# Kernel tuning notes

Measured on AMD Instinct MI355X. Metric: run time of the kernel, lower is better.

Reference implementation:

```python
import jax, jax.numpy as jnp
import numpy as np
from jax import lax

B, T, I, H, N = 8192, 100, 24, 64, 8  # batch, seq_len, input_size, hidden_size, hidden_neurons
H2 = 2 * H


def setup_inputs() -> dict:
    key = jax.random.key(0)
    ks = iter(jax.random.split(key, 80))
    d = {"input_seq": jax.random.normal(next(ks), (B, T, I), jnp.float32)}
    def triple(name, shape):
        d[name + "_mu"] = 0.1 * jax.random.normal(next(ks), shape, jnp.float32)
        d[name + "_rho"] = -6.0 + 0.1 * jax.random.normal(next(ks), shape, jnp.float32)
        d[name + "_eps"] = jax.random.normal(next(ks), shape, jnp.float32)
    # BayesianLSTM params: weight_ih (in, 4H), weight_hh (H, 4H), bias (4H,)
    triple("l1_wih", (I, 4 * H)); triple("l1_whh", (H, 4 * H)); triple("l1_b", (4 * H,))
    triple("l2_wih", (H, 4 * H2)); triple("l2_whh", (H2, 4 * H2)); triple("l2_b", (4 * H2,))
    # BayesianLinear params: weight (out, in), bias (out,)
    triple("fc1_w", (N, H2)); triple("fc1_b", (N,))
    triple("fc2_w", (N, N)); triple("fc2_b", (N,))
    triple("out_w", (1, N)); triple("out_b", (1,))
    return d


def _sample(mu, rho, eps):
    # blitz reparameterization: sigma = log1p(exp(rho))
    return mu + jnp.log1p(jnp.exp(rho)) * eps


def _lstm(x, wih, whh, b):
    # x: [B, T, in]; returns full hidden sequence [B, T, Hn]; gate order i,f,g,o
    Hn = whh.shape[0]
    xg = jnp.einsum('bti,ig->btg', x, wih) + b  # precompute input projection
    def step(carry, xg_t):
        h, c = carry
        gates = xg_t + h @ whh
        i, f, g, o = jnp.split(gates, 4, axis=-1)
        c = jax.nn.sigmoid(f) * c + jax.nn.sigmoid(i) * jnp.tanh(g)
        h = jax.nn.sigmoid(o) * jnp.tanh(c)
        return (h, c), h
    h0 = jnp.zeros((x.shape[0], Hn), x.dtype)
    _, hs = lax.scan(step, (h0, h0), jnp.swapaxes(xg, 0, 1))
    return jnp.swapaxes(hs, 0, 1)


def _forward(input_seq,
             l1_wih_mu, l1_wih_rho, l1_wih_eps, l1_whh_mu, l1_whh_rho, l1_whh_eps,
             l1_b_mu, l1_b_rho, l1_b_eps,
             l2_wih_mu, l2_wih_rho, l2_wih_eps, l2_whh_mu, l2_whh_rho, l2_whh_eps,
             l2_b_mu, l2_b_rho, l2_b_eps,
             fc1_w_mu, fc1_w_rho, fc1_w_eps, fc1_b_mu, fc1_b_rho, fc1_b_eps,
             fc2_w_mu, fc2_w_rho, fc2_w_eps, fc2_b_mu, fc2_b_rho, fc2_b_eps,
             out_w_mu, out_w_rho, out_w_eps, out_b_mu, out_b_rho, out_b_eps):
    w1i = _sample(l1_wih_mu, l1_wih_rho, l1_wih_eps)
    w1h = _sample(l1_whh_mu, l1_whh_rho, l1_whh_eps)
    b1 = _sample(l1_b_mu, l1_b_rho, l1_b_eps)
    w2i = _sample(l2_wih_mu, l2_wih_rho, l2_wih_eps)
    w2h = _sample(l2_whh_mu, l2_whh_rho, l2_whh_eps)
    b2 = _sample(l2_b_mu, l2_b_rho, l2_b_eps)
    fc1w = _sample(fc1_w_mu, fc1_w_rho, fc1_w_eps); fc1b = _sample(fc1_b_mu, fc1_b_rho, fc1_b_eps)
    fc2w = _sample(fc2_w_mu, fc2_w_rho, fc2_w_eps); fc2b = _sample(fc2_b_mu, fc2_b_rho, fc2_b_eps)
    outw = _sample(out_w_mu, out_w_rho, out_w_eps); outb = _sample(out_b_mu, out_b_rho, out_b_eps)

    h1 = _lstm(input_seq, w1i, w1h, b1)      # [B, T, H]
    h2 = _lstm(h1, w2i, w2h, b2)             # [B, T, 2H]
    out = h2[:, -1, :]                       # [B, 2H]
    x = jax.nn.relu(out @ fc1w.T + fc1b)
    x = jax.nn.relu(x @ fc2w.T + fc2b)
    y = x @ outw.T + outb                    # [B, 1]
    return y.reshape(-1)


def reference(input_seq,
              l1_wih_mu, l1_wih_rho, l1_wih_eps, l1_whh_mu, l1_whh_rho, l1_whh_eps,
              l1_b_mu, l1_b_rho, l1_b_eps,
              l2_wih_mu, l2_wih_rho, l2_wih_eps, l2_whh_mu, l2_whh_rho, l2_whh_eps,
              l2_b_mu, l2_b_rho, l2_b_eps,
              fc1_w_mu, fc1_w_rho, fc1_w_eps, fc1_b_mu, fc1_b_rho, fc1_b_eps,
              fc2_w_mu, fc2_w_rho, fc2_w_eps, fc2_b_mu, fc2_b_rho, fc2_b_eps,
              out_w_mu, out_w_rho, out_w_eps, out_b_mu, out_b_rho, out_b_eps):
    return _forward(input_seq,
                    l1_wih_mu, l1_wih_rho, l1_wih_eps, l1_whh_mu, l1_whh_rho, l1_whh_eps,
                    l1_b_mu, l1_b_rho, l1_b_eps,
                    l2_wih_mu, l2_wih_rho, l2_wih_eps, l2_whh_mu, l2_whh_rho, l2_whh_eps,
                    l2_b_mu, l2_b_rho, l2_b_eps,
                    fc1_w_mu, fc1_w_rho, fc1_w_eps, fc1_b_mu, fc1_b_rho, fc1_b_eps,
                    fc2_w_mu, fc2_w_rho, fc2_w_eps, fc2_b_mu, fc2_b_rho, fc2_b_eps,
                    out_w_mu, out_w_rho, out_w_eps, out_b_mu, out_b_rho, out_b_eps)
```

## Files before the change

kernel.cpp:

```cpp
#include <hip/hip_runtime.h>
#include <math.h>


typedef __attribute__((ext_vector_type(8))) short short8;
typedef __attribute__((ext_vector_type(4))) float f32x4;

#define MFMA16(a, b, c) __builtin_amdgcn_mfma_f32_16x16x32_bf16((a), (b), (c), 0, 0, 0)

#define WS_W1G_OFF 196608
#define WS_WF_OFF  245760

struct SampParams {
  const float* w1i[3]; const float* w1h[3]; const float* b1[3];
  const float* w2i[3]; const float* w2h[3]; const float* b2[3];
  const float* f1w[3]; const float* f1b[3];
  const float* f2w[3]; const float* f2b[3];
  const float* ow[3];  const float* ob[3];
  short* W2S; short* W1G; float* WF;
};

struct LstmParams {
  const float* input;
  const short* W2S; const short* W1G; const float* WF;
  float* out;
};

__device__ __forceinline__ float softplus_fast(float x) {
  float e = __builtin_amdgcn_exp2f(1.44269504f * x);
  return 0.69314718f * __builtin_amdgcn_logf(1.0f + e);
}

__device__ __forceinline__ float samp(const float* const q[3], int idx) {
  return q[0][idx] + softplus_fast(q[1][idx]) * q[2][idx];
}

__device__ __forceinline__ short f2bf(float f) {
  unsigned u = __float_as_uint(f);
  unsigned r = (u + 0x7FFFu + ((u >> 16) & 1u)) >> 16;
  return (short)r;
}

__device__ __forceinline__ unsigned cvt_pk_bf16(float lo, float hi) {
  unsigned r;
  asm("v_cvt_pk_bf16_f32 %0, %1, %2" : "=v"(r) : "v"(lo), "v"(hi));
  return r;
}

__device__ __forceinline__ void lstm_elem(float gi, float gf, float gg, float go,
                                          float& c, float& h) {
  float A = 1.0f + __builtin_amdgcn_exp2f(-1.44269504f * gi);
  float B = 1.0f + __builtin_amdgcn_exp2f(-1.44269504f * gf);
  float r = __builtin_amdgcn_rcpf(A * B);
  float si = r * B;
  float sf = r * A;
  float C = 1.0f + __builtin_amdgcn_exp2f(2.88539008f * gg);
  float D = 1.0f + __builtin_amdgcn_exp2f(-1.44269504f * go);
  float r2 = __builtin_amdgcn_rcpf(C * D);
  float tg = 1.0f - 2.0f * (r2 * D);
  float so = r2 * C;
  float cn = sf * c + si * tg;
  c = cn;
  float E = 1.0f + __builtin_amdgcn_exp2f(2.88539008f * cn);
  h = so * (1.0f - 2.0f * __builtin_amdgcn_rcpf(E));
}

__global__ __launch_bounds__(256) void sample_kernel(SampParams p)
{
  int i = blockIdx.x * 256 + threadIdx.x;
  if (i < 12288) {
    int tid = i & 511, gg = (i >> 9) & 3, kk = i >> 11;
    int quad = (tid >> 4) & 3, col = tid & 15, v0 = (tid >> 6) * 16;
    int c = gg * 128 + v0 + col;
    short8 v;
#pragma unroll
    for (int j = 0; j < 8; ++j) {
      int k = kk * 32 + quad * 8 + j;
      float x = (k < 64) ? samp(p.w2i, k * 512 + c) : samp(p.w2h, (k - 64) * 512 + c);
      v[j] = f2bf(x);
    }
    *(short8*)&p.W2S[i * 8] = v;
  } else if (i < 15360) {
    int u = i - 12288;
    int slice = u >> 8, n = u & 255;
    int k0 = (slice >> 2) * 32 + (slice & 3) * 8;
    short8 v;
#pragma unroll
    for (int j = 0; j < 8; ++j) {
      int k = k0 + j;
      float x = 0.0f;
      if (k < 24)       x = samp(p.w1i, k * 256 + n);
      else if (k >= 32) x = samp(p.w1h, (k - 32) * 256 + n);
      v[j] = f2bf(x);
    }
    *(short8*)&p.W1G[u * 8] = v;
  } else if (i < 17241) {
    int u = i - 15360;
    float x;
    if (u < 256)       x = samp(p.b1,  u);
    else if (u < 768)  x = samp(p.b2,  u - 256);
    else if (u < 1792) x = samp(p.f1w, u - 768);
    else if (u < 1856) x = samp(p.f2w, u - 1792);
    else if (u < 1864) x = samp(p.f1b, u - 1856);
    else if (u < 1872) x = samp(p.f2b, u - 1864);
    else if (u < 1880) x = samp(p.ow,  u - 1872);
    else               x = samp(p.ob,  0);
    p.WF[u] = x;
  }
}


__global__ __launch_bounds__(512, 2)
void blstm_kernel(LstmParams p)
{
  __shared__ __align__(16) unsigned char pool[79872];
  short* const W1L = (short*)pool;
  short* const A1b = (short*)(pool + 49152);
  short* const A2b = (short*)(pool + 62464);

  const int tid  = threadIdx.x;
  const int w    = tid >> 6;
  const int l    = tid & 63;
  const int quad = l >> 4;
  const int col  = l & 15;
  const int b0   = blockIdx.x * 32;

  const int wq = w & 3;
  const int mh = w >> 2;
  const int v0 = w * 16;

  const short8* const W2v = (const short8*)p.W2S;
  short8 w2r[24];
#pragma unroll
  for (int f = 0; f < 24; ++f) w2r[f] = W2v[f * 512 + tid];

#pragma unroll
  for (int r = 0; r < 6; ++r) {
    short8 v = *(const short8*)&p.W1G[(r * 512 + tid) * 8];
    *(short8*)&W1L[(r * 512 + tid) * 8] = v;
  }

  float b1v[4], b2v[4];
#pragma unroll
  for (int g = 0; g < 4; ++g) b1v[g] = p.WF[g * 64 + wq * 16 + col];
#pragma unroll
  for (int g = 0; g < 4; ++g) b2v[g] = p.WF[256 + g * 128 + v0 + col];

  for (int i = tid; i < 6656; i += 512) A1b[i] = 0;
  for (int i = tid; i < 8704; i += 512) A2b[i] = 0;
  __syncthreads();

  int xr = 0, xi = 0;
  const bool xln = tid < 384;
  const float* xptr = p.input;
  if (xln) {
    int e = tid * 2; xr = e / 24; xi = e - xr * 24;
    const float* base = p.input + (size_t)(b0 + xr) * 2400 + xi;
    float2 xv = *(const float2*)base;
    *(unsigned*)&A1b[xr * 104 + xi] = cvt_pk_bf16(xv.x, xv.y);
    xptr = base + 24;
  }
  __syncthreads();

  float c1a[4]  = {0.f, 0.f, 0.f, 0.f};
  float c2a[2][4] = {{0.f,0.f,0.f,0.f},{0.f,0.f,0.f,0.f}};
  float hf2[2][4];

  const int a1rd = (mh * 16 + col) * 104;

  auto step = [&](const short* __restrict__ A1r, const short* __restrict__ A2r,
                  short* __restrict__ A1w, short* __restrict__ A2w, bool dox) {
    const bool do_x = dox && xln;
    float2 xv;
    if (do_x) xv = *(const float2*)xptr;

    short8 aA0 = *(const short8*)&A1r[a1rd +      quad * 8];
    short8 aA1 = *(const short8*)&A1r[a1rd + 32 + quad * 8];
    short8 aA2 = *(const short8*)&A1r[a1rd + 64 + quad * 8];
    f32x4 g1[4];
#pragma unroll
    for (int g = 0; g < 4; ++g) {
      f32x4 acc = (f32x4){b1v[g], b1v[g], b1v[g], b1v[g]};
      acc = MFMA16(aA0, *(const short8*)&W1L[(((0 * 4 + quad) << 8) + g * 64 + wq * 16 + col) * 8], acc);
      acc = MFMA16(aA1, *(const short8*)&W1L[(((1 * 4 + quad) << 8) + g * 64 + wq * 16 + col) * 8], acc);
      acc = MFMA16(aA2, *(const short8*)&W1L[(((2 * 4 + quad) << 8) + g * 64 + wq * 16 + col) * 8], acc);
      g1[g] = acc;
    }

    {
      float h1v[4];
#pragma unroll
      for (int i = 0; i < 4; ++i)
        lstm_elem(g1[0][i], g1[1][i], g1[2][i], g1[3][i], c1a[i], h1v[i]);
      int base = (mh * 16 + quad * 4) * 104 + 32 + wq * 16 + col;
      unsigned pkA = cvt_pk_bf16(h1v[0], h1v[1]);
      unsigned pkB = cvt_pk_bf16(h1v[2], h1v[3]);
      A1w[base]       = (short)pkA;
      A1w[base + 104] = (short)(pkA >> 16);
      A1w[base + 208] = (short)pkB;
      A1w[base + 312] = (short)(pkB >> 16);
    }
    if (do_x)
      *(unsigned*)&A1w[xr * 104 + xi] = cvt_pk_bf16(xv.x, xv.y);

    f32x4 g2[2][4];
#pragma unroll
    for (int g = 0; g < 4; ++g) {
      g2[0][g] = (f32x4){b2v[g], b2v[g], b2v[g], b2v[g]};
      g2[1][g] = g2[0][g];
    }
#pragma unroll
    for (int kk = 0; kk < 6; ++kk) {
      short8 a0, a1f;
      if (kk < 2) {
        a0  = *(const short8*)&A1r[      col  * 104 + 32 + kk * 32 + quad * 8];
        a1f = *(const short8*)&A1r[(16 + col) * 104 + 32 + kk * 32 + quad * 8];
      } else {
        int o = (kk - 2) * 32 + quad * 8;
        a0  = *(const short8*)&A2r[      col  * 136 + o];
        a1f = *(const short8*)&A2r[(16 + col) * 136 + o];
      }
#pragma unroll
      for (int g = 0; g < 4; ++g) {
        g2[0][g] = MFMA16(a0,  w2r[kk * 4 + g], g2[0][g]);
        g2[1][g] = MFMA16(a1f, w2r[kk * 4 + g], g2[1][g]);
      }
    }

    {
      int u2 = v0 + col;
#pragma unroll
      for (int mi = 0; mi < 2; ++mi) {
        float hv[4];
#pragma unroll
        for (int i = 0; i < 4; ++i) {
          lstm_elem(g2[mi][0][i], g2[mi][1][i], g2[mi][2][i], g2[mi][3][i],
                    c2a[mi][i], hv[i]);
          hf2[mi][i] = hv[i];
        }
        unsigned pkA = cvt_pk_bf16(hv[0], hv[1]);
        unsigned pkB = cvt_pk_bf16(hv[2], hv[3]);
        int base = (mi * 16 + quad * 4) * 136 + u2;
        A2w[base]       = (short)pkA;
        A2w[base + 136] = (short)(pkA >> 16);
        A2w[base + 272] = (short)pkB;
        A2w[base + 408] = (short)(pkB >> 16);
      }
    }
  };

  short* const A1_0 = A1b;            short* const A1_1 = A1b + 3328;
  short* const A2_0 = A2b;            short* const A2_1 = A2b + 4352;

  {
    float2 xv;
    if (xln) xv = *(const float2*)xptr;
    short8 aA0 = *(const short8*)&A1_0[a1rd +      quad * 8];
    short8 aA1 = *(const short8*)&A1_0[a1rd + 32 + quad * 8];
    short8 aA2 = *(const short8*)&A1_0[a1rd + 64 + quad * 8];
    f32x4 g1[4];
#pragma unroll
    for (int g = 0; g < 4; ++g) {
      f32x4 acc = (f32x4){b1v[g], b1v[g], b1v[g], b1v[g]};
      acc = MFMA16(aA0, *(const short8*)&W1L[(((0 * 4 + quad) << 8) + g * 64 + wq * 16 + col) * 8], acc);
      acc = MFMA16(aA1, *(const short8*)&W1L[(((1 * 4 + quad) << 8) + g * 64 + wq * 16 + col) * 8], acc);
      acc = MFMA16(aA2, *(const short8*)&W1L[(((2 * 4 + quad) << 8) + g * 64 + wq * 16 + col) * 8], acc);
      g1[g] = acc;
    }
    float h1v[4];
#pragma unroll
    for (int i = 0; i < 4; ++i)
      lstm_elem(g1[0][i], g1[1][i], g1[2][i], g1[3][i], c1a[i], h1v[i]);
    int base = (mh * 16 + quad * 4) * 104 + 32 + wq * 16 + col;
    unsigned pkA = cvt_pk_bf16(h1v[0], h1v[1]);
    unsigned pkB = cvt_pk_bf16(h1v[2], h1v[3]);
    A1_1[base]       = (short)pkA;
    A1_1[base + 104] = (short)(pkA >> 16);
    A1_1[base + 208] = (short)pkB;
    A1_1[base + 312] = (short)(pkB >> 16);
    if (xln)
      *(unsigned*)&A1_1[xr * 104 + xi] = cvt_pk_bf16(xv.x, xv.y);
    __syncthreads();
    xptr += 24;
  }

  for (int jj = 1; jj <= 99; jj += 2) {
    step(A1_1, A2_1, A1_0, A2_0, jj <= 98);
    __syncthreads();
    xptr += 24;
    step(A1_0, A2_0, A1_1, A2_1, jj + 1 <= 98);
    __syncthreads();
    xptr += 24;
  }

  float* const H2   = (float*)pool;
  float* const FC1W = (float*)(pool + 16896);
  float* const FC2W = (float*)(pool + 20992);
  float* const FB1  = (float*)(pool + 21248);
  float* const FB2  = (float*)(pool + 21280);
  float* const OWp  = (float*)(pool + 21312);
  float* const OBp  = (float*)(pool + 21344);
  float* const X1   = (float*)(pool + 21376);
  float* const X2   = (float*)(pool + 22400);

  {
    int u2 = v0 + col;
#pragma unroll
    for (int mi = 0; mi < 2; ++mi)
#pragma unroll
      for (int i = 0; i < 4; ++i) {
        int row = mi * 16 + quad * 4 + i;
        H2[row * 132 + u2] = hf2[mi][i];
      }
  }
  for (int i = tid; i < 1024; i += 512) FC1W[i] = p.WF[768 + i];
  if (tid < 64)               FC2W[tid]     = p.WF[1792 + tid];
  if (tid >= 64 && tid < 72)  FB1[tid - 64] = p.WF[1856 + tid - 64];
  if (tid >= 72 && tid < 80)  FB2[tid - 72] = p.WF[1864 + tid - 72];
  if (tid >= 80 && tid < 88)  OWp[tid - 80] = p.WF[1872 + tid - 80];
  if (tid == 88)              OBp[0]        = p.WF[1880];
  __syncthreads();

  if (tid < 256) {
    int row = tid >> 3, o = tid & 7;
    float s = FB1[o];
#pragma unroll 8
    for (int k = 0; k < 128; ++k) s += H2[row * 132 + k] * FC1W[o * 128 + k];
    X1[tid] = fmaxf(s, 0.0f);
  }
  __syncthreads();
  if (tid < 256) {
    int row = tid >> 3, o = tid & 7;
    float s = FB2[o];
#pragma unroll
    for (int k = 0; k < 8; ++k) s += X1[row * 8 + k] * FC2W[o * 8 + k];
    X2[tid] = fmaxf(s, 0.0f);
  }
  __syncthreads();
  if (tid < 32) {
    float s = OBp[0];
#pragma unroll
    for (int k = 0; k < 8; ++k) s += X2[tid * 8 + k] * OWp[k];
    p.out[b0 + tid] = s;
  }
}

extern "C" void kernel_launch(void* const* d_in, const int* in_sizes, int n_in,
                              void* d_out, int out_size, void* d_ws, size_t ws_size,
                              hipStream_t stream)
{
  (void)in_sizes; (void)n_in; (void)ws_size; (void)out_size;

  SampParams sp;
  const float** grp[12] = { sp.w1i, sp.w1h, sp.b1, sp.w2i, sp.w2h, sp.b2,
                            sp.f1w, sp.f1b, sp.f2w, sp.f2b, sp.ow, sp.ob };
  int idx = 1;
  for (int t = 0; t < 12; ++t)
    for (int j = 0; j < 3; ++j)
      grp[t][j] = (const float*)d_in[idx++];
  sp.W2S = (short*)d_ws;
  sp.W1G = (short*)((char*)d_ws + WS_W1G_OFF);
  sp.WF  = (float*)((char*)d_ws + WS_WF_OFF);

  LstmParams bp;
  bp.input = (const float*)d_in[0];
  bp.W2S = (const short*)d_ws;
  bp.W1G = (const short*)((char*)d_ws + WS_W1G_OFF);
  bp.WF  = (const float*)((char*)d_ws + WS_WF_OFF);
  bp.out = (float*)d_out;

  sample_kernel<<<dim3(68), dim3(256), 0, stream>>>(sp);
  blstm_kernel<<<dim3(256), dim3(512), 0, stream>>>(bp);
}
```

Before: 400.0 us.

## Prefetch input one step ahead, batch LSTM reciprocals, use LDS-only barriers

Input loads for timestep t+1 are now issued one step early and written the following step, so global-load latency is hidden behind a full recurrence step. The LSTM cell math is restructured to share one reciprocal across all four gates and one across pairs of tanh(c), which cuts transcendental ops on the serial critical path. The cell state is clamped before the exp to avoid overflow. __syncthreads is replaced with an asm barrier that waits only on lgkmcnt, so the barrier does not stall on outstanding global loads. The risks are lower accuracy from the combined reciprocals and a correctness dependence on the custom barrier.

Result: slower. 410.0 us (+2.5%).

```diff
diff --git a/kernel.cpp b/kernel.cpp
--- a/kernel.cpp
+++ b/kernel.cpp
@@ -6,6 +6,8 @@
 typedef __attribute__((ext_vector_type(4))) float f32x4;
 
 #define MFMA16(a, b, c) __builtin_amdgcn_mfma_f32_16x16x32_bf16((a), (b), (c), 0, 0, 0)
+
+#define BARRIER() asm volatile("s_waitcnt lgkmcnt(0)\n\ts_barrier" ::: "memory")
 
 #define WS_W1G_OFF 196608
 #define WS_WF_OFF  245760
@@ -46,22 +48,35 @@
   return r;
 }
 
-__device__ __forceinline__ void lstm_elem(float gi, float gf, float gg, float go,
-                                          float& c, float& h) {
-  float A = 1.0f + __builtin_amdgcn_exp2f(-1.44269504f * gi);
-  float B = 1.0f + __builtin_amdgcn_exp2f(-1.44269504f * gf);
-  float r = __builtin_amdgcn_rcpf(A * B);
-  float si = r * B;
-  float sf = r * A;
-  float C = 1.0f + __builtin_amdgcn_exp2f(2.88539008f * gg);
-  float D = 1.0f + __builtin_amdgcn_exp2f(-1.44269504f * go);
-  float r2 = __builtin_amdgcn_rcpf(C * D);
-  float tg = 1.0f - 2.0f * (r2 * D);
-  float so = r2 * C;
-  float cn = sf * c + si * tg;
-  c = cn;
-  float E = 1.0f + __builtin_amdgcn_exp2f(2.88539008f * cn);
-  h = so * (1.0f - 2.0f * __builtin_amdgcn_rcpf(E));
+__device__ __forceinline__ void lstm_quad(const f32x4 gi, const f32x4 gf,
+                                          const f32x4 gg, const f32x4 go,
+                                          float* c, float* h) {
+  float E[4], so[4];
+#pragma unroll
+  for (int i = 0; i < 4; ++i) {
+    float a  = __builtin_amdgcn_exp2f(-1.44269504f * gi[i]);
+    float b  = __builtin_amdgcn_exp2f(-1.44269504f * gf[i]);
+    float cv = __builtin_amdgcn_exp2f( 2.88539008f * gg[i]);
+    float d  = __builtin_amdgcn_exp2f(-1.44269504f * go[i]);
+    float A = 1.0f + a, B = 1.0f + b, C = 1.0f + cv, D = 1.0f + d;
+    float P = A * B, Q = C * D;
+    float R = __builtin_amdgcn_rcpf(P * Q);
+    float RQ = R * Q, RP = R * P;
+    float si = RQ * B;
+    float sf = RQ * A;
+    float tg = 1.0f - 2.0f * (RP * D);
+    so[i]    = RP * C;
+    float cn = sf * c[i] + si * tg;
+    c[i] = cn;
+    float cc = fminf(fmaxf(cn, -15.0f), 15.0f);
+    E[i] = 1.0f + __builtin_amdgcn_exp2f(2.88539008f * cc);
+  }
+  float R01 = __builtin_amdgcn_rcpf(E[0] * E[1]);
+  float R23 = __builtin_amdgcn_rcpf(E[2] * E[3]);
+  h[0] = so[0] * (1.0f - 2.0f * (R01 * E[1]));
+  h[1] = so[1] * (1.0f - 2.0f * (R01 * E[0]));
+  h[2] = so[2] * (1.0f - 2.0f * (R23 * E[3]));
+  h[3] = so[3] * (1.0f - 2.0f * (R23 * E[2]));
 }
 
 __global__ __launch_bounds__(256) void sample_kernel(SampParams p)
@@ -155,23 +170,24 @@
   if (xln) {
     int e = tid * 2; xr = e / 24; xi = e - xr * 24;
     const float* base = p.input + (size_t)(b0 + xr) * 2400 + xi;
-    float2 xv = *(const float2*)base;
-    *(unsigned*)&A1b[xr * 104 + xi] = cvt_pk_bf16(xv.x, xv.y);
+    float2 xv0 = *(const float2*)base;
+    *(unsigned*)&A1b[xr * 104 + xi] = cvt_pk_bf16(xv0.x, xv0.y);
     xptr = base + 24;
   }
   __syncthreads();
 
-  float c1a[4]  = {0.f, 0.f, 0.f, 0.f};
+  float c1a[4]    = {0.f, 0.f, 0.f, 0.f};
   float c2a[2][4] = {{0.f,0.f,0.f,0.f},{0.f,0.f,0.f,0.f}};
   float hf2[2][4];
 
+  float2 xv_w, xv_n;
+
   const int a1rd = (mh * 16 + col) * 104;
 
   auto step = [&](const short* __restrict__ A1r, const short* __restrict__ A2r,
-                  short* __restrict__ A1w, short* __restrict__ A2w, bool dox) {
-    const bool do_x = dox && xln;
-    float2 xv;
-    if (do_x) xv = *(const float2*)xptr;
+                  short* __restrict__ A1w, short* __restrict__ A2w,
+                  bool w_x, bool l_x) {
+    if (l_x && xln) xv_n = *(const float2*)xptr;
 
     short8 aA0 = *(const short8*)&A1r[a1rd +      quad * 8];
     short8 aA1 = *(const short8*)&A1r[a1rd + 32 + quad * 8];
@@ -188,9 +204,7 @@
 
     {
       float h1v[4];
-#pragma unroll
-      for (int i = 0; i < 4; ++i)
-        lstm_elem(g1[0][i], g1[1][i], g1[2][i], g1[3][i], c1a[i], h1v[i]);
+      lstm_quad(g1[0], g1[1], g1[2], g1[3], c1a, h1v);
       int base = (mh * 16 + quad * 4) * 104 + 32 + wq * 16 + col;
       unsigned pkA = cvt_pk_bf16(h1v[0], h1v[1]);
       unsigned pkB = cvt_pk_bf16(h1v[2], h1v[3]);
@@ -199,8 +213,8 @@
       A1w[base + 208] = (short)pkB;
       A1w[base + 312] = (short)(pkB >> 16);
     }
-    if (do_x)
-      *(unsigned*)&A1w[xr * 104 + xi] = cvt_pk_bf16(xv.x, xv.y);
+    if (w_x && xln)
+      *(unsigned*)&A1w[xr * 104 + xi] = cvt_pk_bf16(xv_w.x, xv_w.y);
 
     f32x4 g2[2][4];
 #pragma unroll
@@ -231,12 +245,9 @@
 #pragma unroll
       for (int mi = 0; mi < 2; ++mi) {
         float hv[4];
-#pragma unroll
-        for (int i = 0; i < 4; ++i) {
-          lstm_elem(g2[mi][0][i], g2[mi][1][i], g2[mi][2][i], g2[mi][3][i],
-                    c2a[mi][i], hv[i]);
-          hf2[mi][i] = hv[i];
-        }
+        lstm_quad(g2[mi][0], g2[mi][1], g2[mi][2], g2[mi][3], c2a[mi], hv);
+#pragma unroll
+        for (int i = 0; i < 4; ++i) hf2[mi][i] = hv[i];
         unsigned pkA = cvt_pk_bf16(hv[0], hv[1]);
         unsigned pkB = cvt_pk_bf16(hv[2], hv[3]);
         int base = (mi * 16 + quad * 4) * 136 + u2;
@@ -246,14 +257,17 @@
         A2w[base + 408] = (short)(pkB >> 16);
       }
     }
+    xv_w = xv_n;
   };
 
   short* const A1_0 = A1b;            short* const A1_1 = A1b + 3328;
   short* const A2_0 = A2b;            short* const A2_1 = A2b + 4352;
 
   {
-    float2 xv;
-    if (xln) xv = *(const float2*)xptr;
+    if (xln) {
+      xv_w = *(const float2*)xptr;
+      xv_n = *(const float2*)(xptr + 24);
+    }
     short8 aA0 = *(const short8*)&A1_0[a1rd +      quad * 8];
     short8 aA1 = *(const short8*)&A1_0[a1rd + 32 + quad * 8];
     short8 aA2 = *(const short8*)&A1_0[a1rd + 64 + quad * 8];
@@ -267,9 +281,7 @@
       g1[g] = acc;
     }
     float h1v[4];
-#pragma unroll
-    for (int i = 0; i < 4; ++i)
-      lstm_elem(g1[0][i], g1[1][i], g1[2][i], g1[3][i], c1a[i], h1v[i]);
+    lstm_quad(g1[0], g1[1], g1[2], g1[3], c1a, h1v);
     int base = (mh * 16 + quad * 4) * 104 + 32 + wq * 16 + col;
     unsigned pkA = cvt_pk_bf16(h1v[0], h1v[1]);
     unsigned pkB = cvt_pk_bf16(h1v[2], h1v[3]);
@@ -278,17 +290,18 @@
     A1_1[base + 208] = (short)pkB;
     A1_1[base + 312] = (short)(pkB >> 16);
     if (xln)
-      *(unsigned*)&A1_1[xr * 104 + xi] = cvt_pk_bf16(xv.x, xv.y);
-    __syncthreads();
+      *(unsigned*)&A1_1[xr * 104 + xi] = cvt_pk_bf16(xv_w.x, xv_w.y);
+    BARRIER();
+    xv_w = xv_n;
+    xptr += 48;
+  }
+
+  for (int jj = 1; jj <= 99; jj += 2) {
+    step(A1_1, A2_1, A1_0, A2_0, jj <= 98, jj <= 97);
+    BARRIER();
     xptr += 24;
-  }
-
-  for (int jj = 1; jj <= 99; jj += 2) {
-    step(A1_1, A2_1, A1_0, A2_0, jj <= 98);
-    __syncthreads();
-    xptr += 24;
-    step(A1_0, A2_0, A1_1, A2_1, jj + 1 <= 98);
-    __syncthreads();
+    step(A1_0, A2_0, A1_1, A2_1, jj + 1 <= 98, jj + 1 <= 97);
+    BARRIER();
     xptr += 24;
   }
 
```

## Double block to 1024 threads, splitting layer-2 gate work across more waves

Applied to the files above, without the earlier changes.

Blocks grow from 512 to 1024 threads. The first 8 waves compute layer 1, and all 16 waves split the layer-2 recurrence so each wave handles one 16-row half of the batch tile. Half of the layer-2 weights stay in registers, and the other half are reloaded from global memory on every step to relieve register pressure. Biases move to shared memory and the final hidden state gets its own LDS region. The risks are extra per-step global weight traffic, larger LDS use, and launch bounds (1024,4) that may cap registers or fail to fit the LDS budget.

Result: slower. 1.029 ms (+157.2%).

```diff
diff --git a/kernel.cpp b/kernel.cpp
--- a/kernel.cpp
+++ b/kernel.cpp
@@ -109,13 +109,15 @@
 }
 
 
-__global__ __launch_bounds__(512, 2)
+__global__ __launch_bounds__(1024, 4)
 void blstm_kernel(LstmParams p)
 {
-  __shared__ __align__(16) unsigned char pool[79872];
+  __shared__ __align__(16) unsigned char pool[99840];
   short* const W1L = (short*)pool;
   short* const A1b = (short*)(pool + 49152);
   short* const A2b = (short*)(pool + 62464);
+  float* const H2F = (float*)(pool + 79872);
+  float* const BIA = (float*)(pool + 96768);
 
   const int tid  = threadIdx.x;
   const int w    = tid >> 6;
@@ -124,69 +126,103 @@
   const int col  = l & 15;
   const int b0   = blockIdx.x * 32;
 
+  const bool hv = (w < 8);
   const int wq = w & 3;
-  const int mh = w >> 2;
-  const int v0 = w * 16;
+  const int mh = (w >> 2) & 1;
+  const int m2 = w & 1;
+  const int cg = w >> 1;
+  const int u2 = cg * 16 + col;
 
   const short8* const W2v = (const short8*)p.W2S;
-  short8 w2r[24];
-#pragma unroll
-  for (int f = 0; f < 24; ++f) w2r[f] = W2v[f * 512 + tid];
-
-#pragma unroll
-  for (int r = 0; r < 6; ++r) {
-    short8 v = *(const short8*)&p.W1G[(r * 512 + tid) * 8];
-    *(short8*)&W1L[(r * 512 + tid) * 8] = v;
-  }
-
-  float b1v[4], b2v[4];
-#pragma unroll
-  for (int g = 0; g < 4; ++g) b1v[g] = p.WF[g * 64 + wq * 16 + col];
-#pragma unroll
-  for (int g = 0; g < 4; ++g) b2v[g] = p.WF[256 + g * 128 + v0 + col];
-
-  for (int i = tid; i < 6656; i += 512) A1b[i] = 0;
-  for (int i = tid; i < 8704; i += 512) A2b[i] = 0;
+  short8 w2r[12];
+#pragma unroll
+  for (int kk = 0; kk < 6; ++kk)
+#pragma unroll
+    for (int g = 0; g < 2; ++g) {
+    }
+#pragma unroll
+  for (int f = 0; f < 12; ++f) {
+    int kk = f / 2;
+    (void)kk;
+  }
+  short8 w2g[12];
+  const int gp = m2;
+#pragma unroll
+  for (int kk = 0; kk < 6; ++kk)
+#pragma unroll
+    for (int gg = 0; gg < 2; ++gg)
+      w2g[kk * 2 + gg] = W2v[(kk * 4 + (gp * 2 + gg)) * 512 + cg * 64 + l];
+
+#pragma unroll
+  for (int r = 0; r < 3; ++r) {
+    short8 v = *(const short8*)&p.W1G[(r * 1024 + tid) * 8];
+    *(short8*)&W1L[(r * 1024 + tid) * 8] = v;
+  }
+
+  if (tid < 768) BIA[tid] = p.WF[tid];
+
+  for (int i = tid; i < 6656; i += 1024) A1b[i] = 0;
+  for (int i = tid; i < 8704; i += 1024) A2b[i] = 0;
   __syncthreads();
 
   int xr = 0, xi = 0;
-  const bool xln = tid < 384;
+  const int xw = tid - 512;
+  const bool xln = (xw >= 0) && (xw < 384);
   const float* xptr = p.input;
   if (xln) {
-    int e = tid * 2; xr = e / 24; xi = e - xr * 24;
+    int e = xw * 2; xr = e / 24; xi = e - xr * 24;
     const float* base = p.input + (size_t)(b0 + xr) * 2400 + xi;
-    float2 xv = *(const float2*)base;
-    *(unsigned*)&A1b[xr * 104 + xi] = cvt_pk_bf16(xv.x, xv.y);
+    float2 xv0 = *(const float2*)base;
+    *(unsigned*)&A1b[xr * 104 + xi] = cvt_pk_bf16(xv0.x, xv0.y);
     xptr = base + 24;
   }
   __syncthreads();
 
   float c1a[4]  = {0.f, 0.f, 0.f, 0.f};
-  float c2a[2][4] = {{0.f,0.f,0.f,0.f},{0.f,0.f,0.f,0.f}};
-  float hf2[2][4];
+  float c2a[4]  = {0.f, 0.f, 0.f, 0.f};
+
+  const int kk0 = m2 * 3;
+  short8 w2h[12];
+#pragma unroll
+  for (int kk = 0; kk < 3; ++kk)
+#pragma unroll
+    for (int g = 0; g < 4; ++g)
+      w2h[kk * 4 + g] = W2v[((kk + kk0) * 4 + g) * 512 + cg * 64 + l];
+
+  float c2r[4] = {0.f, 0.f, 0.f, 0.f};
 
   const int a1rd = (mh * 16 + col) * 104;
 
   auto step = [&](const short* __restrict__ A1r, const short* __restrict__ A2r,
-                  short* __restrict__ A1w, short* __restrict__ A2w, bool dox) {
+                  short* __restrict__ A1w, short* __restrict__ A2w,
+                  bool dox, bool last) {
     const bool do_x = dox && xln;
     float2 xv;
     if (do_x) xv = *(const float2*)xptr;
 
-    short8 aA0 = *(const short8*)&A1r[a1rd +      quad * 8];
-    short8 aA1 = *(const short8*)&A1r[a1rd + 32 + quad * 8];
-    short8 aA2 = *(const short8*)&A1r[a1rd + 64 + quad * 8];
-    f32x4 g1[4];
-#pragma unroll
-    for (int g = 0; g < 4; ++g) {
-      f32x4 acc = (f32x4){b1v[g], b1v[g], b1v[g], b1v[g]};
-      acc = MFMA16(aA0, *(const short8*)&W1L[(((0 * 4 + quad) << 8) + g * 64 + wq * 16 + col) * 8], acc);
-      acc = MFMA16(aA1, *(const short8*)&W1L[(((1 * 4 + quad) << 8) + g * 64 + wq * 16 + col) * 8], acc);
-      acc = MFMA16(aA2, *(const short8*)&W1L[(((2 * 4 + quad) << 8) + g * 64 + wq * 16 + col) * 8], acc);
-      g1[g] = acc;
-    }
-
-    {
+    short8 w2s[12];
+#pragma unroll
+    for (int kk = 0; kk < 3; ++kk)
+#pragma unroll
+      for (int g = 0; g < 4; ++g)
+        w2s[kk * 4 + g] = W2v[((kk + (3 - kk0)) * 4 + g) * 512 + cg * 64 + l];
+
+    if (hv) {
+      float b1v[4];
+#pragma unroll
+      for (int g = 0; g < 4; ++g) b1v[g] = BIA[g * 64 + wq * 16 + col];
+      short8 aA0 = *(const short8*)&A1r[a1rd +      quad * 8];
+      short8 aA1 = *(const short8*)&A1r[a1rd + 32 + quad * 8];
+      short8 aA2 = *(const short8*)&A1r[a1rd + 64 + quad * 8];
+      f32x4 g1[4];
+#pragma unroll
+      for (int g = 0; g < 4; ++g) {
+        f32x4 acc = (f32x4){b1v[g], b1v[g], b1v[g], b1v[g]};
+        acc = MFMA16(aA0, *(const short8*)&W1L[(((0 * 4 + quad) << 8) + g * 64 + wq * 16 + col) * 8], acc);
+        acc = MFMA16(aA1, *(const short8*)&W1L[(((1 * 4 + quad) << 8) + g * 64 + wq * 16 + col) * 8], acc);
+        acc = MFMA16(aA2, *(const short8*)&W1L[(((2 * 4 + quad) << 8) + g * 64 + wq * 16 + col) * 8], acc);
+        g1[g] = acc;
+      }
       float h1v[4];
 #pragma unroll
       for (int i = 0; i < 4; ++i)
@@ -202,48 +238,53 @@
     if (do_x)
       *(unsigned*)&A1w[xr * 104 + xi] = cvt_pk_bf16(xv.x, xv.y);
 
-    f32x4 g2[2][4];
-#pragma unroll
-    for (int g = 0; g < 4; ++g) {
-      g2[0][g] = (f32x4){b2v[g], b2v[g], b2v[g], b2v[g]};
-      g2[1][g] = g2[0][g];
-    }
-#pragma unroll
-    for (int kk = 0; kk < 6; ++kk) {
-      short8 a0, a1f;
-      if (kk < 2) {
-        a0  = *(const short8*)&A1r[      col  * 104 + 32 + kk * 32 + quad * 8];
-        a1f = *(const short8*)&A1r[(16 + col) * 104 + 32 + kk * 32 + quad * 8];
-      } else {
-        int o = (kk - 2) * 32 + quad * 8;
-        a0  = *(const short8*)&A2r[      col  * 136 + o];
-        a1f = *(const short8*)&A2r[(16 + col) * 136 + o];
-      }
-#pragma unroll
-      for (int g = 0; g < 4; ++g) {
-        g2[0][g] = MFMA16(a0,  w2r[kk * 4 + g], g2[0][g]);
-        g2[1][g] = MFMA16(a1f, w2r[kk * 4 + g], g2[1][g]);
-      }
-    }
-
+    f32x4 g2[4];
     {
-      int u2 = v0 + col;
-#pragma unroll
-      for (int mi = 0; mi < 2; ++mi) {
-        float hv[4];
-#pragma unroll
-        for (int i = 0; i < 4; ++i) {
-          lstm_elem(g2[mi][0][i], g2[mi][1][i], g2[mi][2][i], g2[mi][3][i],
-                    c2a[mi][i], hv[i]);
-          hf2[mi][i] = hv[i];
-        }
-        unsigned pkA = cvt_pk_bf16(hv[0], hv[1]);
-        unsigned pkB = cvt_pk_bf16(hv[2], hv[3]);
-        int base = (mi * 16 + quad * 4) * 136 + u2;
-        A2w[base]       = (short)pkA;
-        A2w[base + 136] = (short)(pkA >> 16);
-        A2w[base + 272] = (short)pkB;
-        A2w[base + 408] = (short)(pkB >> 16);
+      float b2v[4];
+#pragma unroll
+      for (int g = 0; g < 4; ++g) b2v[g] = BIA[256 + g * 128 + u2];
+#pragma unroll
+      for (int g = 0; g < 4; ++g)
+        g2[g] = (f32x4){b2v[g], b2v[g], b2v[g], b2v[g]};
+    }
+    const int arow = (m2 * 16 + col);
+#pragma unroll
+    for (int kk = 0; kk < 3; ++kk) {
+      int kka = kk + kk0;
+      short8 a0;
+      if (kka < 2) a0 = *(const short8*)&A1r[arow * 104 + 32 + kka * 32 + quad * 8];
+      else         a0 = *(const short8*)&A2r[arow * 136 + (kka - 2) * 32 + quad * 8];
+#pragma unroll
+      for (int g = 0; g < 4; ++g)
+        g2[g] = MFMA16(a0, w2h[kk * 4 + g], g2[g]);
+    }
+#pragma unroll
+    for (int kk = 0; kk < 3; ++kk) {
+      int kka = kk + (3 - kk0);
+      short8 a0;
+      if (kka < 2) a0 = *(const short8*)&A1r[arow * 104 + 32 + kka * 32 + quad * 8];
+      else         a0 = *(const short8*)&A2r[arow * 136 + (kka - 2) * 32 + quad * 8];
+#pragma unroll
+      for (int g = 0; g < 4; ++g)
+        g2[g] = MFMA16(a0, w2s[kk * 4 + g], g2[g]);
+    }
+
+    {
+      float hv4[4];
+#pragma unroll
+      for (int i = 0; i < 4; ++i)
+        lstm_elem(g2[0][i], g2[1][i], g2[2][i], g2[3][i], c2r[i], hv4[i]);
+      unsigned pkA = cvt_pk_bf16(hv4[0], hv4[1]);
+      unsigned pkB = cvt_pk_bf16(hv4[2], hv4[3]);
+      int base = (m2 * 16 + quad * 4) * 136 + u2;
+      A2w[base]       = (short)pkA;
+      A2w[base + 136] = (short)(pkA >> 16);
+      A2w[base + 272] = (short)pkB;
+      A2w[base + 408] = (short)(pkB >> 16);
+      if (last) {
+#pragma unroll
+        for (int i = 0; i < 4; ++i)
+          H2F[(m2 * 16 + quad * 4 + i) * 132 + u2] = hv4[i];
       }
     }
   };
@@ -254,29 +295,34 @@
   {
     float2 xv;
     if (xln) xv = *(const float2*)xptr;
-    short8 aA0 = *(const short8*)&A1_0[a1rd +      quad * 8];
-    short8 aA1 = *(const short8*)&A1_0[a1rd + 32 + quad * 8];
-    short8 aA2 = *(const short8*)&A1_0[a1rd + 64 + quad * 8];
-    f32x4 g1[4];
-#pragma unroll
-    for (int g = 0; g < 4; ++g) {
-      f32x4 acc = (f32x4){b1v[g], b1v[g], b1v[g], b1v[g]};
-      acc = MFMA16(aA0, *(const short8*)&W1L[(((0 * 4 + quad) << 8) + g * 64 + wq * 16 + col) * 8], acc);
-      acc = MFMA16(aA1, *(const short8*)&W1L[(((1 * 4 + quad) << 8) + g * 64 + wq * 16 + col) * 8], acc);
-      acc = MFMA16(aA2, *(const short8*)&W1L[(((2 * 4 + quad) << 8) + g * 64 + wq * 16 + col) * 8], acc);
-      g1[g] = acc;
-    }
-    float h1v[4];
-#pragma unroll
-    for (int i = 0; i < 4; ++i)
-      lstm_elem(g1[0][i], g1[1][i], g1[2][i], g1[3][i], c1a[i], h1v[i]);
-    int base = (mh * 16 + quad * 4) * 104 + 32 + wq * 16 + col;
-    unsigned pkA = cvt_pk_bf16(h1v[0], h1v[1]);
-    unsigned pkB = cvt_pk_bf16(h1v[2], h1v[3]);
-    A1_1[base]       = (short)pkA;
-    A1_1[base + 104] = (short)(pkA >> 16);
-    A1_1[base + 208] = (short)pkB;
-    A1_1[base + 312] = (short)(pkB >> 16);
+    if (hv) {
+      float b1v[4];
+#pragma unroll
+      for (int g = 0; g < 4; ++g) b1v[g] = BIA[g * 64 + wq * 16 + col];
+      short8 aA0 = *(const short8*)&A1_0[a1rd +      quad * 8];
+      short8 aA1 = *(const short8*)&A1_0[a1rd + 32 + quad * 8];
+      short8 aA2 = *(const short8*)&A1_0[a1rd + 64 + quad * 8];
+      f32x4 g1[4];
+#pragma unroll
+      for (int g = 0; g < 4; ++g) {
+        f32x4 acc = (f32x4){b1v[g], b1v[g], b1v[g], b1v[g]};
+        acc = MFMA16(aA0, *(const short8*)&W1L[(((0 * 4 + quad) << 8) + g * 64 + wq * 16 + col) * 8], acc);
+        acc = MFMA16(aA1, *(const short8*)&W1L[(((1 * 4 + quad) << 8) + g * 64 + wq * 16 + col) * 8], acc);
+        acc = MFMA16(aA2, *(const short8*)&W1L[(((2 * 4 + quad) << 8) + g * 64 + wq * 16 + col) * 8], acc);
+        g1[g] = acc;
+      }
+      float h1v[4];
+#pragma unroll
+      for (int i = 0; i < 4; ++i)
+        lstm_elem(g1[0][i], g1[1][i], g1[2][i], g1[3][i], c1a[i], h1v[i]);
+      int base = (mh * 16 + quad * 4) * 104 + 32 + wq * 16 + col;
+      unsigned pkA = cvt_pk_bf16(h1v[0], h1v[1]);
+      unsigned pkB = cvt_pk_bf16(h1v[2], h1v[3]);
+      A1_1[base]       = (short)pkA;
+      A1_1[base + 104] = (short)(pkA >> 16);
+      A1_1[base + 208] = (short)pkB;
+      A1_1[base + 312] = (short)(pkB >> 16);
+    }
     if (xln)
       *(unsigned*)&A1_1[xr * 104 + xi] = cvt_pk_bf16(xv.x, xv.y);
     __syncthreads();
@@ -284,15 +330,14 @@
   }
 
   for (int jj = 1; jj <= 99; jj += 2) {
-    step(A1_1, A2_1, A1_0, A2_0, jj <= 98);
+    step(A1_1, A2_1, A1_0, A2_0, jj <= 98, false);
     __syncthreads();
     xptr += 24;
-    step(A1_0, A2_0, A1_1, A2_1, jj + 1 <= 98);
+    step(A1_0, A2_0, A1_1, A2_1, jj + 1 <= 98, jj + 1 == 100);
     __syncthreads();
     xptr += 24;
   }
 
-  float* const H2   = (float*)pool;
   float* const FC1W = (float*)(pool + 16896);
   float* const FC2W = (float*)(pool + 20992);
   float* const FB1  = (float*)(pool + 21248);
@@ -302,17 +347,7 @@
   float* const X1   = (float*)(pool + 21376);
   float* const X2   = (float*)(pool + 22400);
 
-  {
-    int u2 = v0 + col;
-#pragma unroll
-    for (int mi = 0; mi < 2; ++mi)
-#pragma unroll
-      for (int i = 0; i < 4; ++i) {
-        int row = mi * 16 + quad * 4 + i;
-        H2[row * 132 + u2] = hf2[mi][i];
-      }
-  }
-  for (int i = tid; i < 1024; i += 512) FC1W[i] = p.WF[768 + i];
+  if (tid < 1024) FC1W[tid] = p.WF[768 + tid];
   if (tid < 64)               FC2W[tid]     = p.WF[1792 + tid];
   if (tid >= 64 && tid < 72)  FB1[tid - 64] = p.WF[1856 + tid - 64];
   if (tid >= 72 && tid < 80)  FB2[tid - 72] = p.WF[1864 + tid - 72];
@@ -324,7 +359,7 @@
     int row = tid >> 3, o = tid & 7;
     float s = FB1[o];
 #pragma unroll 8
-    for (int k = 0; k < 128; ++k) s += H2[row * 132 + k] * FC1W[o * 128 + k];
+    for (int k = 0; k < 128; ++k) s += H2F[row * 132 + k] * FC1W[o * 128 + k];
     X1[tid] = fmaxf(s, 0.0f);
   }
   __syncthreads();
@@ -369,5 +404,5 @@
   bp.out = (float*)d_out;
 
   sample_kernel<<<dim3(68), dim3(256), 0, stream>>>(sp);
-  blstm_kernel<<<dim3(256), dim3(512), 0, stream>>>(bp);
-}
+  blstm_kernel<<<dim3(256), dim3(1024), 0, stream>>>(bp);
+}
```
